# Kernel optimization log

Measured on AMD Instinct MI355X. Metric: run time of the kernel, lower is better.

## Reference

```python
import jax, jax.numpy as jnp
import numpy as np

INPUT_DIM = 512
HIDDEN_DIM = 1024

def setup_inputs() -> dict:
    key = jax.random.key(0)
    k1, k2, k3, k4 = jax.random.split(key, 4)
    D, H = INPUT_DIM, HIDDEN_DIM
    x = jax.random.normal(k1, (64, 512, D), dtype=jnp.float32)
    # Lecun-normal-ish init like flax Linear defaults
    W_in = jax.random.normal(k2, (D, 3 * H), dtype=jnp.float32) / np.sqrt(D)
    b_in = jnp.zeros((3 * H,), dtype=jnp.float32)
    W_h = jax.random.normal(k3, (H, 3 * H), dtype=jnp.float32) / np.sqrt(H)
    return {"x": x, "W_in": W_in, "b_in": b_in, "W_h": W_h}

def reference(x, W_in, b_in, W_h):
    B, S, D = x.shape
    H = W_h.shape[0]
    # Precompute input projection for all timesteps: (S, B, 3H)
    x_proj = jnp.einsum('bsd,dk->sbk', x, W_in) + b_in
    h0 = jnp.zeros((B, H), dtype=x.dtype)

    def gru_step(h, x_t):
        hx = h @ W_h  # (B, 3H)
        z = jax.nn.sigmoid(x_t[:, :H] + hx[:, :H])
        r = jax.nn.sigmoid(x_t[:, H:2 * H] + hx[:, H:2 * H])
        n = jnp.tanh(x_t[:, 2 * H:] + r * hx[:, 2 * H:])
        h_new = (1 - z) * n + z * h
        return h_new, h_new

    h_final, h_all = jax.lax.scan(gru_step, h0, x_proj)
    h_all = jnp.transpose(h_all, (1, 0, 2))  # (B, S, H)
    return (h_final, h_all)
```

## Files before the change

### kernel.cpp

```cpp
#include <hip/hip_runtime.h>
#include <math.h>

#define D_IN   512
#define HID    1024
#define SEQ    512
#define NBATCH 64
#define K3     3072
#define KTOT   1536
#define WB_ELEMS (K3 * KTOT)
#define NBLK   256
#define BLOCK_T 768

typedef __attribute__((ext_vector_type(8))) short short8;
typedef __attribute__((ext_vector_type(4))) float f32x4;
typedef __attribute__((ext_vector_type(4))) unsigned u32x4;
typedef _Float16 half8 __attribute__((ext_vector_type(8)));

#define MFMA_BF16(a, b, c) __builtin_amdgcn_mfma_f32_16x16x32_bf16((a), (b), (c), 0, 0, 0)
#define MFMA_F16(a, b, c)  __builtin_amdgcn_mfma_f32_16x16x32_f16((a), (b), (c), 0, 0, 0)

__global__ __launch_bounds__(256) void build_wt(const float* __restrict__ Win,
                                                const float* __restrict__ Wh,
                                                unsigned short* __restrict__ WBh,
                                                unsigned short* __restrict__ WBl) {
    int idx = blockIdx.x * 256 + threadIdx.x;
    if (idx >= WB_ELEMS) return;
    int k   = idx % KTOT;
    int col = idx / KTOT;
    float v = (k < D_IN) ? Win[(size_t)k * K3 + col]
                         : Wh[(size_t)(k - D_IN) * K3 + col];
    unsigned short hb, lb;
    if (k < D_IN) {
        __bf16 h = (__bf16)v;
        hb = __builtin_bit_cast(unsigned short, h);
        lb = __builtin_bit_cast(unsigned short, (__bf16)(v - (float)h));
    } else {
        _Float16 h = (_Float16)v;
        hb = __builtin_bit_cast(unsigned short, h);
        lb = __builtin_bit_cast(unsigned short, (_Float16)(v - (float)h));
    }
    WBh[idx] = hb;
    WBl[idx] = lb;
}

__device__ __forceinline__ void cvt8(const f32x4& v0, const f32x4& v1,
                                     short8& ahi, short8& alo) {
    float af[8] = {v0[0], v0[1], v0[2], v0[3], v1[0], v1[1], v1[2], v1[3]};
    #pragma unroll
    for (int j = 0; j < 8; ++j) {
        __bf16 hb = (__bf16)af[j];
        __bf16 lb = (__bf16)(af[j] - (float)hb);
        ahi[j] = __builtin_bit_cast(short, hb);
        alo[j] = __builtin_bit_cast(short, lb);
    }
}

__global__ __attribute__((amdgpu_waves_per_eu(3, 3)))
__launch_bounds__(BLOCK_T) void gru_persist(
        const float* __restrict__ x, const float* __restrict__ bin,
        const unsigned short* __restrict__ WBh, const unsigned short* __restrict__ WBl,
        float* __restrict__ out, unsigned short* __restrict__ hx3,
        unsigned* __restrict__ flags) {
    __shared__ float red[2][12][3][4][64];
    float* hall = out + NBATCH * HID;

    const int tid = threadIdx.x;
    const int l   = tid & 63;
    const int w   = tid >> 6;
    const int xcd = blockIdx.x & 7;
    const int j   = blockIdx.x >> 3;
    const int nb  = xcd + 8 * (j >> 2);
    const int mq  = j & 3;
    const int cb  = nb * 16;

    const int m    = mq * 16 + (l & 15);
    const int koff = (l >> 4) * 8;
    const int colz = cb + (l & 15);
    const bool isH = (w < 8);
    const int kbase = isH ? (D_IN + 128 * w) : (128 * (w - 8));

    const unsigned* fpal = flags + ((size_t)mq * 64 + 8 * w) * 4 + (l & 31);

    short8 Bh[3][4], Bl[3][4];
    #pragma unroll
    for (int g = 0; g < 3; ++g) {
        #pragma unroll
        for (int s = 0; s < 4; ++s) {
            const size_t o = (size_t)(colz + g * HID) * KTOT + kbase + 32 * s + koff;
            Bh[g][s] = *(const short8*)(WBh + o);
            Bl[g][s] = *(const short8*)(WBl + o);
        }
    }
    #pragma unroll
    for (int g = 0; g < 3; ++g) {
        #pragma unroll
        for (int s = 0; s < 4; ++s) {
            asm volatile("" : "+v"(Bh[g][s]));
            asm volatile("" : "+v"(Bl[g][s]));
        }
    }

    const int r2 = tid >> 6;
    const int l2 = tid & 63;
    const int be = mq * 16 + (l2 >> 4) * 4 + r2;
    const int ce = cb + (l2 & 15);
    float bz = 0.f, br = 0.f, bnb = 0.f, hreg = 0.f;
    unsigned* fprod = flags + ((size_t)mq * 64 + nb) * 4 + r2;
    const int p_w  = nb >> 3;
    const int p_si = (nb & 7) >> 1;
    const int p_g  = ((nb & 1) << 1) | ((l2 >> 3) & 1);
    const int p_e  = l2 & 7;
    const int p_b  = (l2 >> 4) * 4 + r2;
    const size_t p_off = (size_t)((p_si * 4 + p_g) * 16 + p_b) * 8 + p_e;
    if (tid < 256) {
        bz  = bin[ce];
        br  = bin[HID + ce];
        bnb = bin[2 * HID + ce];
    }
    asm volatile("" : "+v"(bz), "+v"(br), "+v"(bnb));

    for (int t = 0; t < SEQ; ++t) {
        f32x4 aZ = {0.f,0.f,0.f,0.f}, aR = {0.f,0.f,0.f,0.f}, aN = {0.f,0.f,0.f,0.f};

        if (isH) {
            if (t > 0) {
                const unsigned tagexp = (unsigned)t;
                const unsigned short* hp = hx3
                    + ((size_t)(((t - 1) & 1) * 4 + mq) * 8 + w) * 2048
                    + (size_t)l * 8;
                u32x4 q0 = {0,0,0,0}, q1 = {0,0,0,0}, q2 = {0,0,0,0}, q3 = {0,0,0,0};
                unsigned need = 0xFu;
                while (true) {
                    unsigned f;
                    asm volatile("global_load_dword %0, %1, off sc0 sc1\n\t"
                                 "s_waitcnt vmcnt(0)"
                                 : "=v"(f) : "v"(fpal));
                    unsigned long long rdy = __ballot(f >= tagexp);
                    if ((need & 1u) && (((rdy >> 0)  & 0xFFull) == 0xFFull)) {
                        asm volatile("global_load_dwordx4 %0, %1, off sc0 sc1"
                                     : "=&v"(q0) : "v"(hp));
                        need &= ~1u;
                    }
                    if ((need & 2u) && (((rdy >> 8)  & 0xFFull) == 0xFFull)) {
                        asm volatile("global_load_dwordx4 %0, %1, off offset:1024 sc0 sc1"
                                     : "=&v"(q1) : "v"(hp));
                        need &= ~2u;
                    }
                    if ((need & 4u) && (((rdy >> 16) & 0xFFull) == 0xFFull)) {
                        asm volatile("global_load_dwordx4 %0, %1, off offset:2048 sc0 sc1"
                                     : "=&v"(q2) : "v"(hp));
                        need &= ~4u;
                    }
                    if ((need & 8u) && (((rdy >> 24) & 0xFFull) == 0xFFull)) {
                        asm volatile("global_load_dwordx4 %0, %1, off offset:3072 sc0 sc1"
                                     : "=&v"(q3) : "v"(hp));
                        need &= ~8u;
                    }
                    if (!need) break;
                    __builtin_amdgcn_s_sleep(1);
                }
                asm volatile("s_waitcnt vmcnt(0)"
                             : "+v"(q0), "+v"(q1), "+v"(q2), "+v"(q3));
                __builtin_amdgcn_sched_barrier(0);
                #define SUBT16(si, q) { \
                    half8 ah = __builtin_bit_cast(half8, (q)); \
                    aZ = MFMA_F16(ah, __builtin_bit_cast(half8, Bh[0][si]), aZ); \
                    aZ = MFMA_F16(ah, __builtin_bit_cast(half8, Bl[0][si]), aZ); \
                    aR = MFMA_F16(ah, __builtin_bit_cast(half8, Bh[1][si]), aR); \
                    aR = MFMA_F16(ah, __builtin_bit_cast(half8, Bl[1][si]), aR); \
                    aN = MFMA_F16(ah, __builtin_bit_cast(half8, Bh[2][si]), aN); \
                    aN = MFMA_F16(ah, __builtin_bit_cast(half8, Bl[2][si]), aN); }
                SUBT16(0, q0)
                SUBT16(1, q1)
                SUBT16(2, q2)
                SUBT16(3, q3)
                #undef SUBT16
            }
        } else {
            const float* xp = x + ((size_t)m * SEQ + t) * D_IN + kbase + koff;
            #pragma unroll
            for (int s = 0; s < 4; ++s) {
                f32x4 v0 = *(const f32x4*)(xp + 32 * s);
                f32x4 v1 = *(const f32x4*)(xp + 32 * s + 4);
                short8 ahi, alo;
                cvt8(v0, v1, ahi, alo);
                aZ = MFMA_BF16(ahi, Bh[0][s], aZ); aZ = MFMA_BF16(ahi, Bl[0][s], aZ);
                aZ = MFMA_BF16(alo, Bh[0][s], aZ);
                aR = MFMA_BF16(ahi, Bh[1][s], aR); aR = MFMA_BF16(ahi, Bl[1][s], aR);
                aR = MFMA_BF16(alo, Bh[1][s], aR);
                aN = MFMA_BF16(ahi, Bh[2][s], aN); aN = MFMA_BF16(ahi, Bl[2][s], aN);
                aN = MFMA_BF16(alo, Bh[2][s], aN);
            }
        }

        const int buf = t & 1;
        #pragma unroll
        for (int r = 0; r < 4; ++r) {
            red[buf][w][0][r][l] = aZ[r];
            red[buf][w][1][r][l] = aR[r];
            red[buf][w][2][r][l] = aN[r];
        }
        __syncthreads();

        if (tid < 256) {
            float sz = 0.f, sr = 0.f, snx = 0.f, snh = 0.f;
            #pragma unroll
            for (int wv = 0; wv < 8; ++wv) {
                sz  += red[buf][wv][0][r2][l2];
                sr  += red[buf][wv][1][r2][l2];
                snh += red[buf][wv][2][r2][l2];
            }
            #pragma unroll
            for (int wv = 8; wv < 12; ++wv) {
                sz  += red[buf][wv][0][r2][l2];
                sr  += red[buf][wv][1][r2][l2];
                snx += red[buf][wv][2][r2][l2];
            }
            float z   = 1.f / (1.f + __expf(-(sz + bz)));
            float rr  = 1.f / (1.f + __expf(-(sr + br)));
            float pre = snx + bnb + rr * snh;
            float e2  = __expf(2.f * pre);
            float n   = 1.f - 2.f / (e2 + 1.f);
            float h   = (1.f - z) * n + z * hreg;
            hreg = h;

            unsigned hv = (unsigned)__builtin_bit_cast(unsigned short, (_Float16)h);
            unsigned short* hxp = hx3
                + ((size_t)((t & 1) * 4 + mq) * 8 + p_w) * 2048 + p_off;
            asm volatile("global_store_short %0, %1, off sc0 sc1"
                         :: "v"(hxp), "v"(hv) : "memory");
            asm volatile("s_waitcnt vmcnt(0)" ::: "memory");
            if ((tid & 63) == 0) {
                unsigned fv = (unsigned)(t + 1);
                asm volatile("global_store_dword %0, %1, off sc0 sc1"
                             :: "v"(fprod), "v"(fv) : "memory");
            }
            hall[((size_t)be * SEQ + t) * HID + ce] = h;
            if (t == SEQ - 1) out[(size_t)be * HID + ce] = h;
        }
    }
}

extern "C" void kernel_launch(void* const* d_in, const int* in_sizes, int n_in,
                              void* d_out, int out_size, void* d_ws, size_t ws_size,
                              hipStream_t stream) {
    const float* x   = (const float*)d_in[0];
    const float* Win = (const float*)d_in[1];
    const float* bin = (const float*)d_in[2];
    const float* Wh  = (const float*)d_in[3];
    float* out = (float*)d_out;

    unsigned short* WBh = (unsigned short*)d_ws;
    unsigned short* WBl = (unsigned short*)d_ws + (size_t)WB_ELEMS;
    const size_t hx_off = ((size_t)2 * WB_ELEMS * sizeof(unsigned short) + (1u << 20))
                          & ~((size_t)(1u << 20) - 1);
    unsigned* flags      = (unsigned*)((char*)d_ws + hx_off);
    unsigned short* hx3  = (unsigned short*)((char*)d_ws + hx_off + 65536);

    hipMemsetAsync(flags, 0, 4096, stream);
    hipLaunchKernelGGL(build_wt, dim3((WB_ELEMS + 255) / 256), dim3(256), 0, stream,
                       Win, Wh, WBh, WBl);
    hipLaunchKernelGGL(gru_persist, dim3(NBLK), dim3(BLOCK_T), 0, stream,
                       x, bin, WBh, WBl, out, hx3, flags);
}
```

Baseline: 2.406 ms.

## Fold input projection into hidden-state waves and prefetch next-step x

Removes the four dedicated input-projection waves, shrinking the block from 12 to 8 waves. Each of the 8 waves now computes its recurrent K-slice plus a 64-wide slice of the input projection, holding extra weight fragments in registers. The next timestep's x tile is loaded right after the reduction, so its latency overlaps the flag wait. This cuts LDS reduction work and block size, but adds register pressure and puts the input MFMAs on the critical path after the h-dependent work.

```diff
diff --git a/kernel.cpp b/kernel.cpp
--- a/kernel.cpp
+++ b/kernel.cpp
@@ -9,7 +9,7 @@
 #define KTOT   1536
 #define WB_ELEMS (K3 * KTOT)
 #define NBLK   256
-#define BLOCK_T 768
+#define BLOCK_T 512
 
 typedef __attribute__((ext_vector_type(8))) short short8;
 typedef __attribute__((ext_vector_type(4))) float f32x4;
@@ -55,13 +55,13 @@
     }
 }
 
-__global__ __attribute__((amdgpu_waves_per_eu(3, 3)))
+__global__ __attribute__((amdgpu_waves_per_eu(2, 2)))
 __launch_bounds__(BLOCK_T) void gru_persist(
         const float* __restrict__ x, const float* __restrict__ bin,
         const unsigned short* __restrict__ WBh, const unsigned short* __restrict__ WBl,
         float* __restrict__ out, unsigned short* __restrict__ hx3,
         unsigned* __restrict__ flags) {
-    __shared__ float red[2][12][3][4][64];
+    __shared__ float red[2][8][4][4][64];
     float* hall = out + NBATCH * HID;
 
     const int tid = threadIdx.x;
@@ -73,15 +73,15 @@
     const int mq  = j & 3;
     const int cb  = nb * 16;
 
-    const int m    = mq * 16 + (l & 15);
-    const int koff = (l >> 4) * 8;
-    const int colz = cb + (l & 15);
-    const bool isH = (w < 8);
-    const int kbase = isH ? (D_IN + 128 * w) : (128 * (w - 8));
+    const int m      = mq * 16 + (l & 15);
+    const int koff   = (l >> 4) * 8;
+    const int colz   = cb + (l & 15);
+    const int kbase  = D_IN + 128 * w;
+    const int kxbase = 64 * w;
 
     const unsigned* fpal = flags + ((size_t)mq * 64 + 8 * w) * 4 + (l & 31);
 
-    short8 Bh[3][4], Bl[3][4];
+    short8 Bh[3][4], Bl[3][4], Bxh[3][2], Bxl[3][2];
     #pragma unroll
     for (int g = 0; g < 3; ++g) {
         #pragma unroll
@@ -90,6 +90,12 @@
             Bh[g][s] = *(const short8*)(WBh + o);
             Bl[g][s] = *(const short8*)(WBl + o);
         }
+        #pragma unroll
+        for (int s = 0; s < 2; ++s) {
+            const size_t o = (size_t)(colz + g * HID) * KTOT + kxbase + 32 * s + koff;
+            Bxh[g][s] = *(const short8*)(WBh + o);
+            Bxl[g][s] = *(const short8*)(WBl + o);
+        }
     }
     #pragma unroll
     for (int g = 0; g < 3; ++g) {
@@ -97,6 +103,11 @@
         for (int s = 0; s < 4; ++s) {
             asm volatile("" : "+v"(Bh[g][s]));
             asm volatile("" : "+v"(Bl[g][s]));
+        }
+        #pragma unroll
+        for (int s = 0; s < 2; ++s) {
+            asm volatile("" : "+v"(Bxh[g][s]));
+            asm volatile("" : "+v"(Bxl[g][s]));
         }
     }
 
@@ -119,78 +130,89 @@
     }
     asm volatile("" : "+v"(bz), "+v"(br), "+v"(bnb));
 
+    f32x4 xv0, xv1, xv2, xv3;
+    {
+        const float* xp = x + (size_t)m * SEQ * D_IN + kxbase + koff;
+        asm volatile(
+            "global_load_dwordx4 %0, %4, off\n\t"
+            "global_load_dwordx4 %1, %4, off offset:16\n\t"
+            "global_load_dwordx4 %2, %4, off offset:128\n\t"
+            "global_load_dwordx4 %3, %4, off offset:144"
+            : "=&v"(xv0), "=&v"(xv1), "=&v"(xv2), "=&v"(xv3)
+            : "v"(xp));
+    }
+
     for (int t = 0; t < SEQ; ++t) {
-        f32x4 aZ = {0.f,0.f,0.f,0.f}, aR = {0.f,0.f,0.f,0.f}, aN = {0.f,0.f,0.f,0.f};
-
-        if (isH) {
-            if (t > 0) {
-                const unsigned tagexp = (unsigned)t;
-                const unsigned short* hp = hx3
-                    + ((size_t)(((t - 1) & 1) * 4 + mq) * 8 + w) * 2048
-                    + (size_t)l * 8;
-                u32x4 q0 = {0,0,0,0}, q1 = {0,0,0,0}, q2 = {0,0,0,0}, q3 = {0,0,0,0};
-                unsigned need = 0xFu;
-                while (true) {
-                    unsigned f;
-                    asm volatile("global_load_dword %0, %1, off sc0 sc1\n\t"
-                                 "s_waitcnt vmcnt(0)"
-                                 : "=v"(f) : "v"(fpal));
-                    unsigned long long rdy = __ballot(f >= tagexp);
-                    if ((need & 1u) && (((rdy >> 0)  & 0xFFull) == 0xFFull)) {
-                        asm volatile("global_load_dwordx4 %0, %1, off sc0 sc1"
-                                     : "=&v"(q0) : "v"(hp));
-                        need &= ~1u;
-                    }
-                    if ((need & 2u) && (((rdy >> 8)  & 0xFFull) == 0xFFull)) {
-                        asm volatile("global_load_dwordx4 %0, %1, off offset:1024 sc0 sc1"
-                                     : "=&v"(q1) : "v"(hp));
-                        need &= ~2u;
-                    }
-                    if ((need & 4u) && (((rdy >> 16) & 0xFFull) == 0xFFull)) {
-                        asm volatile("global_load_dwordx4 %0, %1, off offset:2048 sc0 sc1"
-                                     : "=&v"(q2) : "v"(hp));
-                        need &= ~4u;
-                    }
-                    if ((need & 8u) && (((rdy >> 24) & 0xFFull) == 0xFFull)) {
-                        asm volatile("global_load_dwordx4 %0, %1, off offset:3072 sc0 sc1"
-                                     : "=&v"(q3) : "v"(hp));
-                        need &= ~8u;
-                    }
-                    if (!need) break;
-                    __builtin_amdgcn_s_sleep(1);
+        f32x4 aZ = {0.f,0.f,0.f,0.f}, aR = {0.f,0.f,0.f,0.f};
+        f32x4 aNH = {0.f,0.f,0.f,0.f}, aNX = {0.f,0.f,0.f,0.f};
+
+        if (t > 0) {
+            const unsigned tagexp = (unsigned)t;
+            const unsigned short* hp = hx3
+                + ((size_t)(((t - 1) & 1) * 4 + mq) * 8 + w) * 2048
+                + (size_t)l * 8;
+            u32x4 q0 = {0,0,0,0}, q1 = {0,0,0,0}, q2 = {0,0,0,0}, q3 = {0,0,0,0};
+            unsigned need = 0xFu;
+            while (true) {
+                unsigned f;
+                asm volatile("global_load_dword %0, %1, off sc0 sc1\n\t"
+                             "s_waitcnt vmcnt(0)"
+                             : "=v"(f) : "v"(fpal));
+                unsigned long long rdy = __ballot(f >= tagexp);
+                if ((need & 1u) && (((rdy >> 0)  & 0xFFull) == 0xFFull)) {
+                    asm volatile("global_load_dwordx4 %0, %1, off sc0 sc1"
+                                 : "=&v"(q0) : "v"(hp));
+                    need &= ~1u;
                 }
-                asm volatile("s_waitcnt vmcnt(0)"
-                             : "+v"(q0), "+v"(q1), "+v"(q2), "+v"(q3));
-                __builtin_amdgcn_sched_barrier(0);
-                #define SUBT16(si, q) { \
-                    half8 ah = __builtin_bit_cast(half8, (q)); \
-                    aZ = MFMA_F16(ah, __builtin_bit_cast(half8, Bh[0][si]), aZ); \
-                    aZ = MFMA_F16(ah, __builtin_bit_cast(half8, Bl[0][si]), aZ); \
-                    aR = MFMA_F16(ah, __builtin_bit_cast(half8, Bh[1][si]), aR); \
-                    aR = MFMA_F16(ah, __builtin_bit_cast(half8, Bl[1][si]), aR); \
-                    aN = MFMA_F16(ah, __builtin_bit_cast(half8, Bh[2][si]), aN); \
-                    aN = MFMA_F16(ah, __builtin_bit_cast(half8, Bl[2][si]), aN); }
-                SUBT16(0, q0)
-                SUBT16(1, q1)
-                SUBT16(2, q2)
-                SUBT16(3, q3)
-                #undef SUBT16
+                if ((need & 2u) && (((rdy >> 8)  & 0xFFull) == 0xFFull)) {
+                    asm volatile("global_load_dwordx4 %0, %1, off offset:1024 sc0 sc1"
+                                 : "=&v"(q1) : "v"(hp));
+                    need &= ~2u;
+                }
+                if ((need & 4u) && (((rdy >> 16) & 0xFFull) == 0xFFull)) {
+                    asm volatile("global_load_dwordx4 %0, %1, off offset:2048 sc0 sc1"
+                                 : "=&v"(q2) : "v"(hp));
+                    need &= ~4u;
+                }
+                if ((need & 8u) && (((rdy >> 24) & 0xFFull) == 0xFFull)) {
+                    asm volatile("global_load_dwordx4 %0, %1, off offset:3072 sc0 sc1"
+                                 : "=&v"(q3) : "v"(hp));
+                    need &= ~8u;
+                }
+                if (!need) break;
+                __builtin_amdgcn_s_sleep(1);
             }
-        } else {
-            const float* xp = x + ((size_t)m * SEQ + t) * D_IN + kbase + koff;
-            #pragma unroll
-            for (int s = 0; s < 4; ++s) {
-                f32x4 v0 = *(const f32x4*)(xp + 32 * s);
-                f32x4 v1 = *(const f32x4*)(xp + 32 * s + 4);
-                short8 ahi, alo;
-                cvt8(v0, v1, ahi, alo);
-                aZ = MFMA_BF16(ahi, Bh[0][s], aZ); aZ = MFMA_BF16(ahi, Bl[0][s], aZ);
-                aZ = MFMA_BF16(alo, Bh[0][s], aZ);
-                aR = MFMA_BF16(ahi, Bh[1][s], aR); aR = MFMA_BF16(ahi, Bl[1][s], aR);
-                aR = MFMA_BF16(alo, Bh[1][s], aR);
-                aN = MFMA_BF16(ahi, Bh[2][s], aN); aN = MFMA_BF16(ahi, Bl[2][s], aN);
-                aN = MFMA_BF16(alo, Bh[2][s], aN);
-            }
+            asm volatile("s_waitcnt vmcnt(0)"
+                         : "+v"(q0), "+v"(q1), "+v"(q2), "+v"(q3));
+            __builtin_amdgcn_sched_barrier(0);
+            #define SUBT16(si, q) { \
+                half8 ah = __builtin_bit_cast(half8, (q)); \
+                aZ  = MFMA_F16(ah, __builtin_bit_cast(half8, Bh[0][si]), aZ); \
+                aZ  = MFMA_F16(ah, __builtin_bit_cast(half8, Bl[0][si]), aZ); \
+                aR  = MFMA_F16(ah, __builtin_bit_cast(half8, Bh[1][si]), aR); \
+                aR  = MFMA_F16(ah, __builtin_bit_cast(half8, Bl[1][si]), aR); \
+                aNH = MFMA_F16(ah, __builtin_bit_cast(half8, Bh[2][si]), aNH); \
+                aNH = MFMA_F16(ah, __builtin_bit_cast(half8, Bl[2][si]), aNH); }
+            SUBT16(0, q0)
+            SUBT16(1, q1)
+            SUBT16(2, q2)
+            SUBT16(3, q3)
+            #undef SUBT16
+        }
+
+        asm volatile("s_waitcnt vmcnt(0)"
+                     : "+v"(xv0), "+v"(xv1), "+v"(xv2), "+v"(xv3));
+        __builtin_amdgcn_sched_barrier(0);
+        #pragma unroll
+        for (int s = 0; s < 2; ++s) {
+            short8 ahi, alo;
+            cvt8((s == 0) ? xv0 : xv2, (s == 0) ? xv1 : xv3, ahi, alo);
+            aZ  = MFMA_BF16(ahi, Bxh[0][s], aZ);  aZ  = MFMA_BF16(ahi, Bxl[0][s], aZ);
+            aZ  = MFMA_BF16(alo, Bxh[0][s], aZ);
+            aR  = MFMA_BF16(ahi, Bxh[1][s], aR);  aR  = MFMA_BF16(ahi, Bxl[1][s], aR);
+            aR  = MFMA_BF16(alo, Bxh[1][s], aR);
+            aNX = MFMA_BF16(ahi, Bxh[2][s], aNX); aNX = MFMA_BF16(ahi, Bxl[2][s], aNX);
+            aNX = MFMA_BF16(alo, Bxh[2][s], aNX);
         }
 
         const int buf = t & 1;
@@ -198,23 +220,22 @@
         for (int r = 0; r < 4; ++r) {
             red[buf][w][0][r][l] = aZ[r];
             red[buf][w][1][r][l] = aR[r];
-            red[buf][w][2][r][l] = aN[r];
+            red[buf][w][2][r][l] = aNH[r];
+            red[buf][w][3][r][l] = aNX[r];
         }
         __syncthreads();
 
+        const int tp = (t + 1 < SEQ) ? t + 1 : SEQ - 1;
+        const float* xpn = x + ((size_t)m * SEQ + tp) * D_IN + kxbase + koff;
+
         if (tid < 256) {
-            float sz = 0.f, sr = 0.f, snx = 0.f, snh = 0.f;
+            float sz = 0.f, sr = 0.f, snh = 0.f, snx = 0.f;
             #pragma unroll
             for (int wv = 0; wv < 8; ++wv) {
                 sz  += red[buf][wv][0][r2][l2];
                 sr  += red[buf][wv][1][r2][l2];
                 snh += red[buf][wv][2][r2][l2];
-            }
-            #pragma unroll
-            for (int wv = 8; wv < 12; ++wv) {
-                sz  += red[buf][wv][0][r2][l2];
-                sr  += red[buf][wv][1][r2][l2];
-                snx += red[buf][wv][2][r2][l2];
+                snx += red[buf][wv][3][r2][l2];
             }
             float z   = 1.f / (1.f + __expf(-(sz + bz)));
             float rr  = 1.f / (1.f + __expf(-(sr + br)));
@@ -235,8 +256,23 @@
                 asm volatile("global_store_dword %0, %1, off sc0 sc1"
                              :: "v"(fprod), "v"(fv) : "memory");
             }
+            asm volatile(
+                "global_load_dwordx4 %0, %4, off\n\t"
+                "global_load_dwordx4 %1, %4, off offset:16\n\t"
+                "global_load_dwordx4 %2, %4, off offset:128\n\t"
+                "global_load_dwordx4 %3, %4, off offset:144"
+                : "=&v"(xv0), "=&v"(xv1), "=&v"(xv2), "=&v"(xv3)
+                : "v"(xpn));
             hall[((size_t)be * SEQ + t) * HID + ce] = h;
             if (t == SEQ - 1) out[(size_t)be * HID + ce] = h;
+        } else {
+            asm volatile(
+                "global_load_dwordx4 %0, %4, off\n\t"
+                "global_load_dwordx4 %1, %4, off offset:16\n\t"
+                "global_load_dwordx4 %2, %4, off offset:128\n\t"
+                "global_load_dwordx4 %3, %4, off offset:144"
+                : "=&v"(xv0), "=&v"(xv1), "=&v"(xv2), "=&v"(xv3)
+                : "v"(xpn));
         }
     }
 }
```

Result: slower. 2.762 ms (+14.8%).
